# Kernel tuning notes

Hardware: AMD Instinct MI355X
Metric: run time of the kernel (lower is better)

The kernel has to match this reference:

```python
import jax, jax.numpy as jnp
import numpy as np

NUM_HEADS = 32
KV_HEADS = 8
HEAD_DIM = 128
ROPE_BASE = 10000.0

def apply_rope(x):
    # x: [B, H, S, D]
    B, H, S, D = x.shape
    inv_freq = 1.0 / (ROPE_BASE ** (jnp.arange(0, D, 2, dtype=jnp.float32) / D))  # [D/2]
    t = jnp.arange(S, dtype=jnp.float32)
    freqs = jnp.einsum('s,d->sd', t, inv_freq)                 # [S, D/2]
    emb = jnp.concatenate([freqs, freqs], axis=-1)             # [S, D]
    cos = jnp.cos(emb)[None, None, :, :].astype(x.dtype)
    sin = jnp.sin(emb)[None, None, :, :].astype(x.dtype)
    x1, x2 = x[..., : D // 2], x[..., D // 2 :]
    rotated = jnp.concatenate([-x2, x1], axis=-1)
    return x * cos + rotated * sin

def setup_inputs() -> dict:
    key = jax.random.key(0)
    ks = jax.random.split(key, 6)
    B, S, H = 1, 2048, 4096
    scale = 1.0 / np.sqrt(H)
    return {
        'hidden_states': jax.random.normal(ks[0], (B, S, H), jnp.float32),
        'attention_mask': jnp.zeros((B, S), jnp.float32),
        'Wq': jax.random.normal(ks[1], (H, NUM_HEADS * HEAD_DIM), jnp.float32) * scale,
        'Wk': jax.random.normal(ks[2], (H, KV_HEADS * HEAD_DIM), jnp.float32) * scale,
        'Wv': jax.random.normal(ks[3], (H, KV_HEADS * HEAD_DIM), jnp.float32) * scale,
        'Wo': jax.random.normal(ks[4], (NUM_HEADS * HEAD_DIM, H), jnp.float32) * scale,
    }

def reference(hidden_states, attention_mask, Wq, Wk, Wv, Wo):
    B, S, _ = hidden_states.shape
    groups = NUM_HEADS // KV_HEADS
    q = (hidden_states @ Wq).reshape(B, S, NUM_HEADS, HEAD_DIM).transpose(0, 2, 1, 3)  # [B,H,S,D]
    k = (hidden_states @ Wk).reshape(B, S, KV_HEADS, HEAD_DIM).transpose(0, 2, 1, 3)   # [B,KV,S,D]
    v = (hidden_states @ Wv).reshape(B, S, KV_HEADS, HEAD_DIM).transpose(0, 2, 1, 3)
    q = apply_rope(q)
    k = apply_rope(k)
    # GQA: repeat kv heads to match query heads
    k = jnp.repeat(k, groups, axis=1)  # [B,H,S,D]
    v = jnp.repeat(v, groups, axis=1)
    scale = 1.0 / jnp.sqrt(jnp.asarray(HEAD_DIM, q.dtype))
    scores = jnp.einsum('bhqd,bhkd->bhqk', q, k) * scale       # [B,H,S,S]
    scores = scores + attention_mask[:, None, None, :]
    attn = jax.nn.softmax(scores, axis=-1)
    out = jnp.einsum('bhqk,bhkd->bhqd', attn, v)               # [B,H,S,D]
    out = out.transpose(0, 2, 1, 3).reshape(B, S, NUM_HEADS * HEAD_DIM)
    return out @ Wo
```

## Files before the change

### kernel.cpp

```cpp
#include <hip/hip_runtime.h>
#include <hip/hip_bf16.h>

typedef __bf16 bf16_t;
typedef __bf16 bf16x8 __attribute__((ext_vector_type(8)));
typedef float f32x4 __attribute__((ext_vector_type(4)));

__device__ __forceinline__ void gload_lds16(const void* g, void* l) {
  __builtin_amdgcn_global_load_lds((const __attribute__((address_space(1))) void*)g,
                                   (__attribute__((address_space(3))) void*)l, 16, 0, 0);
}

__global__ __launch_bounds__(256) void cvt_bf16_kernel(const float* __restrict__ src,
                                                       bf16_t* __restrict__ dst, int n8) {
  int i = blockIdx.x * 256 + threadIdx.x;
  if (i >= n8) return;
  const float4* s4 = (const float4*)src;
  float4 a = s4[2 * i], b = s4[2 * i + 1];
  bf16x8 o;
  o[0] = (bf16_t)a.x; o[1] = (bf16_t)a.y; o[2] = (bf16_t)a.z; o[3] = (bf16_t)a.w;
  o[4] = (bf16_t)b.x; o[5] = (bf16_t)b.y; o[6] = (bf16_t)b.z; o[7] = (bf16_t)b.w;
  *(bf16x8*)(dst + 8 * (size_t)i) = o;
}

__global__ __launch_bounds__(256) void trcvt_kernel(const float* __restrict__ src,
                                                    bf16_t* __restrict__ dst, int R, int C) {
  __shared__ float tile[32][33];
  int c0 = blockIdx.x * 32, r0 = blockIdx.y * 32;
  int tx = threadIdx.x, ty = threadIdx.y;
#pragma unroll
  for (int i = 0; i < 4; ++i)
    tile[ty + i * 8][tx] = src[(size_t)(r0 + ty + i * 8) * C + c0 + tx];
  __syncthreads();
#pragma unroll
  for (int i = 0; i < 4; ++i)
    dst[(size_t)(c0 + ty + i * 8) * R + r0 + tx] = (bf16_t)tile[tx][ty + i * 8];
}

__global__ __launch_bounds__(256) void trb_kernel(const bf16_t* __restrict__ src,
                                                  bf16_t* __restrict__ dst, int R, int C) {
  __shared__ bf16_t tile[32][33];
  int c0 = blockIdx.x * 32, r0 = blockIdx.y * 32;
  int tx = threadIdx.x, ty = threadIdx.y;
#pragma unroll
  for (int i = 0; i < 4; ++i)
    tile[ty + i * 8][tx] = src[(size_t)(r0 + ty + i * 8) * C + c0 + tx];
  __syncthreads();
#pragma unroll
  for (int i = 0; i < 4; ++i)
    dst[(size_t)(c0 + ty + i * 8) * R + r0 + tx] = tile[tx][ty + i * 8];
}

__global__ __launch_bounds__(256) void rope_tab_kernel(float* __restrict__ cosT,
                                                       float* __restrict__ sinT) {
  int i = blockIdx.x * 256 + threadIdx.x;
  int s = i >> 6, d = i & 63;
  float ang = (float)s * powf(10000.0f, -(float)d * (1.0f / 64.0f));
  cosT[i] = cosf(ang);
  sinT[i] = sinf(ang);
}

template <int MODE>
__global__ __launch_bounds__(256, 2) void gemm_bt_kernel(
    const bf16_t* __restrict__ A, const bf16_t* __restrict__ B0,
    const bf16_t* __restrict__ B1, const float* __restrict__ cosT,
    const float* __restrict__ sinT, bf16_t* __restrict__ Qb,
    bf16_t* __restrict__ Kb, bf16_t* __restrict__ Vb, float* __restrict__ Cout) {
  constexpr int K = 4096;
  constexpr int MT = 16;
  __shared__ alignas(16) unsigned char sAB[32768];
  unsigned char* sA = sAB;
  unsigned char* sB = sAB + 16384;
  const int bx = blockIdx.x;
  const int mt = bx % MT, nt = bx / MT;
  const int bm = mt * 128;
  const bf16_t* Bt;
  if (MODE == 0)
    Bt = (nt < 32) ? (B0 + (size_t)nt * 128 * K) : (B1 + (size_t)(nt - 32) * 128 * K);
  else
    Bt = B0 + (size_t)nt * 128 * K;

  const int t = threadIdx.x;
  const int sr = t >> 3;
  const int scol = ((t & 7) ^ (sr & 7)) * 8;
  const bf16_t* aG = A + (size_t)(bm + sr) * K + scol;
  const bf16_t* bG = Bt + (size_t)sr * K + scol;
  unsigned char* aL = sA + t * 16;
  unsigned char* bL = sB + t * 16;

  const int lane = t & 63, w = t >> 6;
  const int lr = lane & 15, lq = lane >> 4;
  const int swz = (lr & 7) << 4;

  f32x4 acc[2][8];
#pragma unroll
  for (int m = 0; m < 2; ++m)
#pragma unroll
    for (int n = 0; n < 8; ++n) acc[m][n] = f32x4{0.f, 0.f, 0.f, 0.f};

  for (int k0 = 0; k0 < K; k0 += 64) {
    __syncthreads();
#pragma unroll
    for (int p = 0; p < 4; ++p) {
      gload_lds16(aG + (size_t)(p * 32) * K + k0, aL + p * 4096);
      gload_lds16(bG + (size_t)(p * 32) * K + k0, bL + p * 4096);
    }
    __syncthreads();
#pragma unroll
    for (int kk = 0; kk < 2; ++kk) {
      bf16x8 af[2], bfr[8];
#pragma unroll
      for (int m = 0; m < 2; ++m)
        af[m] = *(const bf16x8*)(sA + (w * 32 + m * 16 + lr) * 128 +
                                 ((kk * 64 + lq * 16) ^ swz));
#pragma unroll
      for (int n = 0; n < 8; ++n)
        bfr[n] = *(const bf16x8*)(sB + (n * 16 + lr) * 128 +
                                  ((kk * 64 + lq * 16) ^ swz));
#pragma unroll
      for (int m = 0; m < 2; ++m)
#pragma unroll
        for (int n = 0; n < 8; ++n)
          acc[m][n] = __builtin_amdgcn_mfma_f32_16x16x32_bf16(af[m], bfr[n],
                                                              acc[m][n], 0, 0, 0);
    }
  }

  if (MODE == 1) {
#pragma unroll
    for (int m = 0; m < 2; ++m)
#pragma unroll
      for (int n = 0; n < 8; ++n)
#pragma unroll
        for (int r = 0; r < 4; ++r)
          Cout[(size_t)(bm + w * 32 + m * 16 + lq * 4 + r) * 4096 + nt * 128 +
               n * 16 + lr] = acc[m][n][r];
  } else {
    const bool isQ = nt < 32;
    const bool isK = (nt >= 32) && (nt < 40);
    if (isQ || isK) {
      bf16_t* dst = isQ ? Qb : Kb;
      const int ld = isQ ? 4096 : 1024;
      const int col0 = isQ ? nt * 128 : (nt - 32) * 128;
      const float qs = isQ ? 0.08838834764831845f : 1.0f;
#pragma unroll
      for (int m = 0; m < 2; ++m)
#pragma unroll
        for (int n = 0; n < 4; ++n)
#pragma unroll
          for (int r = 0; r < 4; ++r) {
            int srow = bm + w * 32 + m * 16 + lq * 4 + r;
            int d = n * 16 + lr;
            float c = cosT[srow * 64 + d], s = sinT[srow * 64 + d];
            float x1 = acc[m][n][r], x2 = acc[m][n + 4][r];
            dst[(size_t)srow * ld + col0 + d] = (bf16_t)((x1 * c - x2 * s) * qs);
            dst[(size_t)srow * ld + col0 + d + 64] = (bf16_t)((x2 * c + x1 * s) * qs);
          }
    } else {
      const int col0 = (nt - 40) * 128;
#pragma unroll
      for (int m = 0; m < 2; ++m)
#pragma unroll
        for (int n = 0; n < 8; ++n)
#pragma unroll
          for (int r = 0; r < 4; ++r)
            Vb[(size_t)(bm + w * 32 + m * 16 + lq * 4 + r) * 1024 + col0 +
               n * 16 + lr] = (bf16_t)acc[m][n][r];
    }
  }
}

__global__ __launch_bounds__(256, 2) void attn_kernel(
    const bf16_t* __restrict__ Qb, const bf16_t* __restrict__ Kb,
    const bf16_t* __restrict__ Vt, const float* __restrict__ mask,
    bf16_t* __restrict__ Ob) {
  extern __shared__ unsigned char sMem[];
  const int bx = blockIdx.x;
  const int h = bx >> 4, qt = bx & 15;
  const int kvh = h >> 2;
  const int q0 = qt * 128;
  const int t = threadIdx.x, lane = t & 63, w = t >> 6;
  const int lr = lane & 15, lq = lane >> 4;
  const int swz = (lr & 7) << 4;

  bf16x8 qf[2][4];
#pragma unroll
  for (int m = 0; m < 2; ++m)
#pragma unroll
    for (int kk = 0; kk < 4; ++kk)
      qf[m][kk] = *(const bf16x8*)(Qb + (size_t)(q0 + w * 32 + m * 16 + lr) * 4096 +
                                   h * 128 + kk * 32 + lq * 8);

  const int srK = t >> 4;
  const int scK = ((t & 15) ^ (srK & 7)) * 8;
  const bf16_t* kG = Kb + (size_t)srK * 1024 + kvh * 128 + scK;
  const int srV = t >> 3;
  const int scV = ((t & 7) ^ (srV & 7)) * 8;
  const bf16_t* vG = Vt + (size_t)(kvh * 128 + srV) * 2048 + scV;

  auto stage = [&](int c, int kt) {
    unsigned char* kL = sMem + c * 16384 + t * 16;
    unsigned char* vL = sMem + 32768 + c * 16384 + t * 16;
#pragma unroll
    for (int p = 0; p < 4; ++p)
      gload_lds16(kG + (size_t)(kt * 64 + p * 16) * 1024, kL + p * 4096);
#pragma unroll
    for (int p = 0; p < 4; ++p)
      gload_lds16(vG + (size_t)(p * 32) * 2048 + kt * 64, vL + p * 4096);
  };

  f32x4 o[2][8];
#pragma unroll
  for (int m = 0; m < 2; ++m)
#pragma unroll
    for (int n = 0; n < 8; ++n) o[m][n] = f32x4{0.f, 0.f, 0.f, 0.f};
  float mrun[2][4], lp[2][4];
#pragma unroll
  for (int m = 0; m < 2; ++m)
#pragma unroll
    for (int r = 0; r < 4; ++r) { mrun[m][r] = -1e30f; lp[m][r] = 0.f; }

  stage(0, 0);
  __syncthreads();

  for (int kt = 0; kt < 32; ++kt) {
    const int cur = kt & 1;
    if (kt < 31) stage(cur ^ 1, kt + 1);
    const unsigned char* sK = sMem + cur * 16384;
    const unsigned char* sV = sMem + 32768 + cur * 16384;
    unsigned char* sPw = sMem + 65536 + w * 4096;

    f32x4 scf[2][4];
#pragma unroll
    for (int m = 0; m < 2; ++m)
#pragma unroll
      for (int n = 0; n < 4; ++n) scf[m][n] = f32x4{0.f, 0.f, 0.f, 0.f};
    __builtin_amdgcn_s_setprio(1);
#pragma unroll
    for (int kk = 0; kk < 4; ++kk)
#pragma unroll
      for (int n = 0; n < 4; ++n) {
        bf16x8 b = *(const bf16x8*)(sK + (n * 16 + lr) * 256 +
                                    ((kk * 64 + lq * 16) ^ swz));
        scf[0][n] = __builtin_amdgcn_mfma_f32_16x16x32_bf16(qf[0][kk], b, scf[0][n], 0, 0, 0);
        scf[1][n] = __builtin_amdgcn_mfma_f32_16x16x32_bf16(qf[1][kk], b, scf[1][n], 0, 0, 0);
      }
    __builtin_amdgcn_s_setprio(0);

    float mk[4];
#pragma unroll
    for (int n = 0; n < 4; ++n) mk[n] = mask[kt * 64 + n * 16 + lr];

    float al[2][4];
#pragma unroll
    for (int m = 0; m < 2; ++m) {
#pragma unroll
      for (int n = 0; n < 4; ++n)
#pragma unroll
        for (int r = 0; r < 4; ++r) scf[m][n][r] += mk[n];
#pragma unroll
      for (int r = 0; r < 4; ++r) {
        float rm = fmaxf(fmaxf(scf[m][0][r], scf[m][1][r]),
                         fmaxf(scf[m][2][r], scf[m][3][r]));
#pragma unroll
        for (int off = 8; off > 0; off >>= 1) rm = fmaxf(rm, __shfl_xor(rm, off));
        float nm = fmaxf(mrun[m][r], rm);
        al[m][r] = __expf(mrun[m][r] - nm);
        mrun[m][r] = nm;
      }
      float ps[4] = {0.f, 0.f, 0.f, 0.f};
#pragma unroll
      for (int n = 0; n < 4; ++n)
#pragma unroll
        for (int r = 0; r < 4; ++r) {
          float p = __expf(scf[m][n][r] - mrun[m][r]);
          scf[m][n][r] = p;
          ps[r] += p;
        }
#pragma unroll
      for (int r = 0; r < 4; ++r) lp[m][r] = lp[m][r] * al[m][r] + ps[r];
#pragma unroll
      for (int n = 0; n < 4; ++n)
#pragma unroll
        for (int r = 0; r < 4; ++r) {
          int prow = lq * 4 + r;
          *(bf16_t*)(sPw + m * 2048 + prow * 128 +
                     (((n * 16 + lr) * 2) ^ ((prow & 7) << 4))) = (bf16_t)scf[m][n][r];
        }
#pragma unroll
      for (int n = 0; n < 8; ++n)
#pragma unroll
        for (int r = 0; r < 4; ++r) o[m][n][r] *= al[m][r];
    }

    bf16x8 pa[2][2];
#pragma unroll
    for (int m = 0; m < 2; ++m)
#pragma unroll
      for (int kk = 0; kk < 2; ++kk)
        pa[m][kk] = *(const bf16x8*)(sPw + m * 2048 + lr * 128 +
                                     ((kk * 64 + lq * 16) ^ swz));
    __builtin_amdgcn_s_setprio(1);
#pragma unroll
    for (int kk = 0; kk < 2; ++kk)
#pragma unroll
      for (int n = 0; n < 8; ++n) {
        bf16x8 vb = *(const bf16x8*)(sV + (n * 16 + lr) * 128 +
                                     ((kk * 64 + lq * 16) ^ swz));
        o[0][n] = __builtin_amdgcn_mfma_f32_16x16x32_bf16(pa[0][kk], vb, o[0][n], 0, 0, 0);
        o[1][n] = __builtin_amdgcn_mfma_f32_16x16x32_bf16(pa[1][kk], vb, o[1][n], 0, 0, 0);
      }
    __builtin_amdgcn_s_setprio(0);
    __syncthreads();
  }

  float inv[2][4];
#pragma unroll
  for (int m = 0; m < 2; ++m)
#pragma unroll
    for (int r = 0; r < 4; ++r) {
      float l = lp[m][r];
#pragma unroll
      for (int off = 8; off > 0; off >>= 1) l += __shfl_xor(l, off);
      inv[m][r] = 1.0f / l;
    }
#pragma unroll
  for (int m = 0; m < 2; ++m)
#pragma unroll
    for (int n = 0; n < 8; ++n)
#pragma unroll
      for (int r = 0; r < 4; ++r)
        Ob[(size_t)(q0 + w * 32 + m * 16 + lq * 4 + r) * 4096 + h * 128 + n * 16 + lr] =
            (bf16_t)(o[m][n][r] * inv[m][r]);
}

extern "C" void kernel_launch(void* const* d_in, const int* in_sizes, int n_in,
                              void* d_out, int out_size, void* d_ws, size_t ws_size,
                              hipStream_t stream) {
  const float* hidden = (const float*)d_in[0];
  const float* mask = (const float*)d_in[1];
  const float* Wq = (const float*)d_in[2];
  const float* Wk = (const float*)d_in[3];
  const float* Wv = (const float*)d_in[4];
  const float* Wo = (const float*)d_in[5];
  float* out = (float*)d_out;
  char* ws = (char*)d_ws;

  bf16_t* hB   = (bf16_t*)(ws + 0);
  bf16_t* Wqt  = (bf16_t*)(ws + 16777216);
  bf16_t* Wkvt = (bf16_t*)(ws + 50331648);
  bf16_t* Wot  = (bf16_t*)(ws + 67108864);
  bf16_t* Qb   = (bf16_t*)(ws + 100663296);
  bf16_t* Kb   = (bf16_t*)(ws + 117440512);
  bf16_t* Vb   = (bf16_t*)(ws + 121634816);
  bf16_t* Vt   = (bf16_t*)(ws + 125829120);
  bf16_t* Ob   = (bf16_t*)(ws + 130023424);
  float*  cosT = (float*)(ws + 146800640);
  float*  sinT = (float*)(ws + 147324928);

  hipFuncSetAttribute((const void*)attn_kernel,
                      hipFuncAttributeMaxDynamicSharedMemorySize, 81920);

  cvt_bf16_kernel<<<4096, 256, 0, stream>>>(hidden, hB, 1048576);
  trcvt_kernel<<<dim3(128, 128), dim3(32, 8), 0, stream>>>(Wq, Wqt, 4096, 4096);
  trcvt_kernel<<<dim3(32, 128), dim3(32, 8), 0, stream>>>(Wk, Wkvt, 4096, 1024);
  trcvt_kernel<<<dim3(32, 128), dim3(32, 8), 0, stream>>>(Wv, Wkvt + (size_t)1024 * 4096, 4096, 1024);
  trcvt_kernel<<<dim3(128, 128), dim3(32, 8), 0, stream>>>(Wo, Wot, 4096, 4096);
  rope_tab_kernel<<<512, 256, 0, stream>>>(cosT, sinT);
  gemm_bt_kernel<0><<<768, 256, 0, stream>>>(hB, Wqt, Wkvt, cosT, sinT, Qb, Kb, Vb, nullptr);
  trb_kernel<<<dim3(32, 64), dim3(32, 8), 0, stream>>>(Vb, Vt, 2048, 1024);
  attn_kernel<<<512, 256, 81920, stream>>>(Qb, Kb, Vt, mask, Ob);
  gemm_bt_kernel<1><<<512, 256, 0, stream>>>(Ob, Wot, nullptr, nullptr, nullptr,
                                             nullptr, nullptr, nullptr, out);
}
```

Baseline: 365.0 us.

## Replace QKV projection GEMM with 256x256-tile, 8-wave, ping-pong pipelined kernel

The fused QKV projection moves from 128x128 tiles with 256 threads to a 256x256 tile with 512 threads and 128KB of dynamic LDS. The main loop double-buffers LDS with global_load_lds, splits each K-step into four MFMA quadrants with barriers, and raises wave priority around the MFMA blocks. The Wq/Wk transposes now permute rows within each head so that each wave's N slice holds the matching RoPE pairs (d and d+64) for the fused RoPE epilogue. The goal is more data reuse per tile and better overlap of loads with MFMA. The cost is only 192 blocks, which may leave some CUs idle on a 256-CU part, plus much higher LDS and register pressure.

```diff
diff --git a/kernel.cpp b/kernel.cpp
--- a/kernel.cpp
+++ b/kernel.cpp
@@ -36,6 +36,25 @@
     dst[(size_t)(c0 + ty + i * 8) * R + r0 + tx] = (bf16_t)tile[tx][ty + i * 8];
 }
 
+__global__ __launch_bounds__(256) void trcvt_perm_kernel(const float* __restrict__ src,
+                                                         bf16_t* __restrict__ dst, int R, int C) {
+  __shared__ float tile[32][33];
+  int c0 = blockIdx.x * 32, r0 = blockIdx.y * 32;
+  int tx = threadIdx.x, ty = threadIdx.y;
+#pragma unroll
+  for (int i = 0; i < 4; ++i)
+    tile[ty + i * 8][tx] = src[(size_t)(r0 + ty + i * 8) * C + c0 + tx];
+  __syncthreads();
+#pragma unroll
+  for (int i = 0; i < 4; ++i) {
+    int rc = c0 + ty + i * 8;
+    int dd = rc & 127;
+    int q = (dd & 15) + ((dd & 16)) + ((dd >> 5) & 1 ? 64 : 0) + ((dd >> 6) ? 32 : 0);
+    int r_out = (rc & ~127) | q;
+    dst[(size_t)r_out * R + r0 + tx] = (bf16_t)tile[tx][ty + i * 8];
+  }
+}
+
 __global__ __launch_bounds__(256) void trb_kernel(const bf16_t* __restrict__ src,
                                                   bf16_t* __restrict__ dst, int R, int C) {
   __shared__ bf16_t tile[32][33];
@@ -59,12 +78,190 @@
   sinT[i] = sinf(ang);
 }
 
-template <int MODE>
-__global__ __launch_bounds__(256, 2) void gemm_bt_kernel(
+__global__ __launch_bounds__(512, 2) void proj_gemm_kernel(
+    const bf16_t* __restrict__ A, const bf16_t* __restrict__ Wqt,
+    const bf16_t* __restrict__ Wkvt, const float* __restrict__ cosT,
+    const float* __restrict__ sinT, bf16_t* __restrict__ Qb,
+    bf16_t* __restrict__ Kb, bf16_t* __restrict__ Vb) {
+  constexpr int K = 4096;
+  extern __shared__ unsigned char sMem[];
+  const int bx = blockIdx.x;
+  const int mt = bx & 7, nt = bx >> 3;
+  const int bm = mt * 256;
+  const bf16_t* Btb = (nt < 16) ? (Wqt + (size_t)nt * 256 * K)
+                                : (Wkvt + (size_t)(nt - 16) * 256 * K);
+
+  const int t = threadIdx.x;
+  const int rowU = t >> 2;
+  const int cole = ((t & 3) * 8) ^ ((rowU & 8) ? 16 : 0);
+  const bf16_t* aS = A + (size_t)(bm + rowU) * K + cole;
+  const bf16_t* bS = Btb + (size_t)rowU * K + cole;
+
+  const int lane = t & 63, w = t >> 6;
+  const int wm = w >> 2, wn = w & 3;
+  const int lr = lane & 15, lq = lane >> 4;
+  const int colb = (lq * 16) ^ ((lr & 8) ? 32 : 0);
+
+  auto stA = [&](int c, int h, int j) {
+    unsigned char* d = sMem + c * 65536 + h * 16384 + t * 16;
+    const bf16_t* g = aS + (size_t)h * 128 * K + j * 64;
+    gload_lds16(g, d);
+    gload_lds16(g + 32, d + 8192);
+  };
+  auto stB = [&](int c, int h, int j) {
+    unsigned char* d = sMem + c * 65536 + 32768 + h * 16384 + t * 16;
+    const bf16_t* g = bS + (size_t)h * 128 * K + j * 64;
+    gload_lds16(g, d);
+    gload_lds16(g + 32, d + 8192);
+  };
+  auto LA = [&](int c, int half, int mi, int kk) {
+    return *(const bf16x8*)(sMem + c * 65536 + wm * 16384 + kk * 8192 +
+                            (half * 64 + mi * 16 + lr) * 64 + colb);
+  };
+  auto LB = [&](int c, int ni, int kk) {
+    return *(const bf16x8*)(sMem + c * 65536 + 32768 + (wn >> 1) * 16384 + kk * 8192 +
+                            ((wn & 1) * 64 + ni * 16 + lr) * 64 + colb);
+  };
+
+  f32x4 acc[8][4];
+#pragma unroll
+  for (int i = 0; i < 8; ++i)
+#pragma unroll
+    for (int n = 0; n < 4; ++n) acc[i][n] = f32x4{0.f, 0.f, 0.f, 0.f};
+
+  stA(0, 0, 0); stA(0, 1, 0); stB(0, 0, 0); stB(0, 1, 0);
+  stB(1, 0, 1); stB(1, 1, 1);
+  asm volatile("s_waitcnt vmcnt(4)" ::: "memory");
+  __builtin_amdgcn_s_barrier();
+  __builtin_amdgcn_sched_barrier(0);
+
+  bf16x8 af[4][2], bf[2][2], bf2[2][2];
+  for (int j = 0; j < 64; ++j) {
+    const int c = j & 1, cn = c ^ 1;
+    const int jp1 = (j + 1 < 64) ? j + 1 : 63;
+    const int jp2 = (j + 2 < 64) ? j + 2 : 63;
+#pragma unroll
+    for (int mi = 0; mi < 4; ++mi)
+#pragma unroll
+      for (int kk = 0; kk < 2; ++kk) af[mi][kk] = LA(c, 0, mi, kk);
+#pragma unroll
+    for (int ni = 0; ni < 2; ++ni)
+#pragma unroll
+      for (int kk = 0; kk < 2; ++kk) bf[ni][kk] = LB(c, ni, kk);
+    stA(cn, 0, jp1);
+    __builtin_amdgcn_s_barrier();
+    __builtin_amdgcn_sched_barrier(0);
+    __builtin_amdgcn_s_setprio(1);
+#pragma unroll
+    for (int kk = 0; kk < 2; ++kk)
+#pragma unroll
+      for (int mi = 0; mi < 4; ++mi)
+#pragma unroll
+        for (int ni = 0; ni < 2; ++ni)
+          acc[mi][ni] = __builtin_amdgcn_mfma_f32_16x16x32_bf16(af[mi][kk], bf[ni][kk],
+                                                                acc[mi][ni], 0, 0, 0);
+    __builtin_amdgcn_s_setprio(0);
+    __builtin_amdgcn_sched_barrier(0);
+    __builtin_amdgcn_s_barrier();
+#pragma unroll
+    for (int ni = 0; ni < 2; ++ni)
+#pragma unroll
+      for (int kk = 0; kk < 2; ++kk) bf2[ni][kk] = LB(c, 2 + ni, kk);
+    stA(cn, 1, jp1);
+    __builtin_amdgcn_s_barrier();
+    __builtin_amdgcn_sched_barrier(0);
+    __builtin_amdgcn_s_setprio(1);
+#pragma unroll
+    for (int kk = 0; kk < 2; ++kk)
+#pragma unroll
+      for (int mi = 0; mi < 4; ++mi)
+#pragma unroll
+        for (int ni = 0; ni < 2; ++ni)
+          acc[mi][2 + ni] = __builtin_amdgcn_mfma_f32_16x16x32_bf16(af[mi][kk], bf2[ni][kk],
+                                                                    acc[mi][2 + ni], 0, 0, 0);
+    __builtin_amdgcn_s_setprio(0);
+    __builtin_amdgcn_sched_barrier(0);
+    __builtin_amdgcn_s_barrier();
+#pragma unroll
+    for (int mi = 0; mi < 4; ++mi)
+#pragma unroll
+      for (int kk = 0; kk < 2; ++kk) af[mi][kk] = LA(c, 1, mi, kk);
+    stB(c, 0, jp2);
+    __builtin_amdgcn_s_barrier();
+    __builtin_amdgcn_sched_barrier(0);
+    __builtin_amdgcn_s_setprio(1);
+#pragma unroll
+    for (int kk = 0; kk < 2; ++kk)
+#pragma unroll
+      for (int mi = 0; mi < 4; ++mi)
+#pragma unroll
+        for (int ni = 0; ni < 2; ++ni)
+          acc[4 + mi][2 + ni] = __builtin_amdgcn_mfma_f32_16x16x32_bf16(
+              af[mi][kk], bf2[ni][kk], acc[4 + mi][2 + ni], 0, 0, 0);
+    __builtin_amdgcn_s_setprio(0);
+    __builtin_amdgcn_sched_barrier(0);
+    __builtin_amdgcn_s_barrier();
+    stB(c, 1, jp2);
+    asm volatile("s_waitcnt vmcnt(4)" ::: "memory");
+    __builtin_amdgcn_s_barrier();
+    __builtin_amdgcn_sched_barrier(0);
+    __builtin_amdgcn_s_setprio(1);
+#pragma unroll
+    for (int kk = 0; kk < 2; ++kk)
+#pragma unroll
+      for (int mi = 0; mi < 4; ++mi)
+#pragma unroll
+        for (int ni = 0; ni < 2; ++ni)
+          acc[4 + mi][ni] = __builtin_amdgcn_mfma_f32_16x16x32_bf16(
+              af[mi][kk], bf[ni][kk], acc[4 + mi][ni], 0, 0, 0);
+    __builtin_amdgcn_s_setprio(0);
+    __builtin_amdgcn_sched_barrier(0);
+    __builtin_amdgcn_s_barrier();
+  }
+
+  if (nt < 20) {
+    const bool isQ = nt < 16;
+    bf16_t* dst = isQ ? Qb : Kb;
+    const int ld = isQ ? 4096 : 1024;
+    const int hh = isQ ? (nt * 2 + (wn >> 1)) : ((nt - 16) * 2 + (wn >> 1));
+    const float qs = isQ ? 0.08838834764831845f : 1.0f;
+    const int dbase = lr + 32 * (wn & 1);
+#pragma unroll
+    for (int half = 0; half < 2; ++half)
+#pragma unroll
+      for (int mi = 0; mi < 4; ++mi)
+#pragma unroll
+        for (int ni = 0; ni < 2; ++ni) {
+          int d = dbase + 16 * ni;
+#pragma unroll
+          for (int r = 0; r < 4; ++r) {
+            int srow = bm + wm * 128 + half * 64 + mi * 16 + lq * 4 + r;
+            float cv = cosT[srow * 64 + d], sv = sinT[srow * 64 + d];
+            float x1 = acc[half * 4 + mi][ni][r], x2 = acc[half * 4 + mi][ni + 2][r];
+            dst[(size_t)srow * ld + hh * 128 + d] = (bf16_t)((x1 * cv - x2 * sv) * qs);
+            dst[(size_t)srow * ld + hh * 128 + d + 64] = (bf16_t)((x2 * cv + x1 * sv) * qs);
+          }
+        }
+  } else {
+    const int col0 = (nt - 20) * 256 + wn * 64;
+#pragma unroll
+    for (int half = 0; half < 2; ++half)
+#pragma unroll
+      for (int mi = 0; mi < 4; ++mi)
+#pragma unroll
+        for (int ni = 0; ni < 4; ++ni)
+#pragma unroll
+          for (int r = 0; r < 4; ++r) {
+            int srow = bm + wm * 128 + half * 64 + mi * 16 + lq * 4 + r;
+            Vb[(size_t)srow * 1024 + col0 + ni * 16 + lr] =
+                (bf16_t)acc[half * 4 + mi][ni][r];
+          }
+  }
+}
+
+__global__ __launch_bounds__(256, 2) void out_gemm_kernel(
     const bf16_t* __restrict__ A, const bf16_t* __restrict__ B0,
-    const bf16_t* __restrict__ B1, const float* __restrict__ cosT,
-    const float* __restrict__ sinT, bf16_t* __restrict__ Qb,
-    bf16_t* __restrict__ Kb, bf16_t* __restrict__ Vb, float* __restrict__ Cout) {
+    float* __restrict__ Cout) {
   constexpr int K = 4096;
   constexpr int MT = 16;
   __shared__ alignas(16) unsigned char sAB[32768];
@@ -73,11 +270,7 @@
   const int bx = blockIdx.x;
   const int mt = bx % MT, nt = bx / MT;
   const int bm = mt * 128;
-  const bf16_t* Bt;
-  if (MODE == 0)
-    Bt = (nt < 32) ? (B0 + (size_t)nt * 128 * K) : (B1 + (size_t)(nt - 32) * 128 * K);
-  else
-    Bt = B0 + (size_t)nt * 128 * K;
+  const bf16_t* Bt = B0 + (size_t)nt * 128 * K;
 
   const int t = threadIdx.x;
   const int sr = t >> 3;
@@ -124,49 +317,14 @@
                                                               acc[m][n], 0, 0, 0);
     }
   }
-
-  if (MODE == 1) {
-#pragma unroll
-    for (int m = 0; m < 2; ++m)
-#pragma unroll
-      for (int n = 0; n < 8; ++n)
-#pragma unroll
-        for (int r = 0; r < 4; ++r)
-          Cout[(size_t)(bm + w * 32 + m * 16 + lq * 4 + r) * 4096 + nt * 128 +
-               n * 16 + lr] = acc[m][n][r];
-  } else {
-    const bool isQ = nt < 32;
-    const bool isK = (nt >= 32) && (nt < 40);
-    if (isQ || isK) {
-      bf16_t* dst = isQ ? Qb : Kb;
-      const int ld = isQ ? 4096 : 1024;
-      const int col0 = isQ ? nt * 128 : (nt - 32) * 128;
-      const float qs = isQ ? 0.08838834764831845f : 1.0f;
-#pragma unroll
-      for (int m = 0; m < 2; ++m)
-#pragma unroll
-        for (int n = 0; n < 4; ++n)
-#pragma unroll
-          for (int r = 0; r < 4; ++r) {
-            int srow = bm + w * 32 + m * 16 + lq * 4 + r;
-            int d = n * 16 + lr;
-            float c = cosT[srow * 64 + d], s = sinT[srow * 64 + d];
-            float x1 = acc[m][n][r], x2 = acc[m][n + 4][r];
-            dst[(size_t)srow * ld + col0 + d] = (bf16_t)((x1 * c - x2 * s) * qs);
-            dst[(size_t)srow * ld + col0 + d + 64] = (bf16_t)((x2 * c + x1 * s) * qs);
-          }
-    } else {
-      const int col0 = (nt - 40) * 128;
-#pragma unroll
-      for (int m = 0; m < 2; ++m)
-#pragma unroll
-        for (int n = 0; n < 8; ++n)
-#pragma unroll
-          for (int r = 0; r < 4; ++r)
-            Vb[(size_t)(bm + w * 32 + m * 16 + lq * 4 + r) * 1024 + col0 +
-               n * 16 + lr] = (bf16_t)acc[m][n][r];
-    }
-  }
+#pragma unroll
+  for (int m = 0; m < 2; ++m)
+#pragma unroll
+    for (int n = 0; n < 8; ++n)
+#pragma unroll
+      for (int r = 0; r < 4; ++r)
+        Cout[(size_t)(bm + w * 32 + m * 16 + lq * 4 + r) * 4096 + nt * 128 +
+             n * 16 + lr] = acc[m][n][r];
 }
 
 __global__ __launch_bounds__(256, 2) void attn_kernel(
@@ -359,16 +517,17 @@
 
   hipFuncSetAttribute((const void*)attn_kernel,
                       hipFuncAttributeMaxDynamicSharedMemorySize, 81920);
+  hipFuncSetAttribute((const void*)proj_gemm_kernel,
+                      hipFuncAttributeMaxDynamicSharedMemorySize, 131072);
 
   cvt_bf16_kernel<<<4096, 256, 0, stream>>>(hidden, hB, 1048576);
-  trcvt_kernel<<<dim3(128, 128), dim3(32, 8), 0, stream>>>(Wq, Wqt, 4096, 4096);
-  trcvt_kernel<<<dim3(32, 128), dim3(32, 8), 0, stream>>>(Wk, Wkvt, 4096, 1024);
+  trcvt_perm_kernel<<<dim3(128, 128), dim3(32, 8), 0, stream>>>(Wq, Wqt, 4096, 4096);
+  trcvt_perm_kernel<<<dim3(32, 128), dim3(32, 8), 0, stream>>>(Wk, Wkvt, 4096, 1024);
   trcvt_kernel<<<dim3(32, 128), dim3(32, 8), 0, stream>>>(Wv, Wkvt + (size_t)1024 * 4096, 4096, 1024);
   trcvt_kernel<<<dim3(128, 128), dim3(32, 8), 0, stream>>>(Wo, Wot, 4096, 4096);
   rope_tab_kernel<<<512, 256, 0, stream>>>(cosT, sinT);
-  gemm_bt_kernel<0><<<768, 256, 0, stream>>>(hB, Wqt, Wkvt, cosT, sinT, Qb, Kb, Vb, nullptr);
+  proj_gemm_kernel<<<192, 512, 131072, stream>>>(hB, Wqt, Wkvt, cosT, sinT, Qb, Kb, Vb);
   trb_kernel<<<dim3(32, 64), dim3(32, 8), 0, stream>>>(Vb, Vt, 2048, 1024);
   attn_kernel<<<512, 256, 81920, stream>>>(Qb, Kb, Vt, mask, Ob);
-  gemm_bt_kernel<1><<<512, 256, 0, stream>>>(Ob, Wot, nullptr, nullptr, nullptr,
-                                             nullptr, nullptr, nullptr, out);
-}
+  out_gemm_kernel<<<512, 256, 0, stream>>>(Ob, Wot, out);
+}
```

After: 352.6 us. 1.04x faster.
